# Performance work log

Measured on AMD Instinct MI355X. Metric: run time of the kernel, lower is better.

Reference implementation:

```python
import jax, jax.numpy as jnp
import numpy as np

D = 1024      # input_dim == attention_dim == num_heads*head_dim
H = 16        # num_heads
HD = 64       # head_dim
FF = 4096     # ff_dim
EPS = 1e-5


def _layernorm(x, gamma, beta):
    mu = jnp.mean(x, axis=-1, keepdims=True)
    var = jnp.var(x, axis=-1, keepdims=True)
    return (x - mu) * jax.lax.rsqrt(var + EPS) * gamma + beta


def setup_inputs() -> dict:
    key = jax.random.key(0)
    ks = jax.random.split(key, 11)
    s_in = 1.0 / np.sqrt(D)
    s_ff = 1.0 / np.sqrt(FF)
    return {
        "x": jax.random.normal(ks[0], (2, 2048, D), dtype=jnp.float32),
        "w_qkv": jax.random.uniform(ks[1], (D, 3 * D), jnp.float32, -s_in, s_in),
        "b_qkv": jax.random.uniform(ks[2], (3 * D,), jnp.float32, -s_in, s_in),
        "w_o": jax.random.uniform(ks[3], (D, D), jnp.float32, -s_in, s_in),
        "b_o": jax.random.uniform(ks[4], (D,), jnp.float32, -s_in, s_in),
        "g1": jnp.ones((D,), jnp.float32),
        "be1": jnp.zeros((D,), jnp.float32),
        "w1": jax.random.uniform(ks[5], (D, FF), jnp.float32, -s_in, s_in),
        "b1": jax.random.uniform(ks[6], (FF,), jnp.float32, -s_in, s_in),
        "w2": jax.random.uniform(ks[7], (FF, D), jnp.float32, -s_ff, s_ff),
        "b2": jax.random.uniform(ks[8], (D,), jnp.float32, -s_ff, s_ff),
        "g2": jnp.ones((D,), jnp.float32),
        "be2": jnp.zeros((D,), jnp.float32),
    }


def reference(x, w_qkv, b_qkv, w_o, b_o, g1, be1, w1, b1, w2, b2, g2, be2):
    N, L, _ = x.shape
    qkv = x @ w_qkv + b_qkv                       # [N, L, 3D]
    q = qkv[..., :D].reshape(N, L, H, HD)
    k = qkv[..., D:2 * D].reshape(N, L, H, HD)
    v = qkv[..., 2 * D:].reshape(N, L, H, HD)
    scores = jnp.einsum('nqhd,nkhd->nhqk', q, k) / np.sqrt(HD)
    attn = jax.nn.softmax(scores, axis=-1)        # [N, H, L, L]
    out = jnp.einsum('nhql,nlhd->nqhd', attn, v).reshape(N, L, D)
    attn_out = out @ w_o + b_o
    # dropout is identity in eval mode
    h = _layernorm(attn_out + x, g1, be1)
    ff = jax.nn.relu(h @ w1 + b1) @ w2 + b2
    return _layernorm(h + ff, g2, be2)
```

## Files before the change

kernel.cpp:

```cpp
#include <hip/hip_runtime.h>
#include <cstddef>
#include <cstdint>

static constexpr int Dm   = 1024;
static constexpr int Hh   = 16;
static constexpr int HDd  = 64;
static constexpr int FFd  = 4096;
static constexpr int Ls   = 2048;
static constexpr int Nb   = 2;
static constexpr int Mrows = Nb * Ls;

typedef short bf16x8 __attribute__((ext_vector_type(8)));
typedef float f32x4  __attribute__((ext_vector_type(4)));

__device__ __forceinline__ ushort f2b(float f) {
    uint32_t u = __builtin_bit_cast(uint32_t, f);
    u = (u + 0x7FFFu + ((u >> 16) & 1u)) >> 16;
    return (ushort)u;
}
__device__ __forceinline__ ushort f2bf(float f) {
    return (ushort)((__builtin_bit_cast(uint32_t, f) + 0x8000u) >> 16);
}
__device__ __forceinline__ float b2f(ushort b) {
    return __builtin_bit_cast(float, (uint32_t)b << 16);
}

__device__ __forceinline__ void gl2lds16(const ushort* g, ushort* l) {
    __builtin_amdgcn_global_load_lds(
        (const __attribute__((address_space(1))) void*)g,
        (__attribute__((address_space(3))) void*)l, 16, 0, 0);
}

__global__ __launch_bounds__(256) void convert_bf16(
    const float* __restrict__ src, ushort* __restrict__ dst, int n)
{
    int i = (blockIdx.x * 256 + threadIdx.x) * 4;
    if (i >= n) return;
    float4 v = *(const float4*)(src + i);
    uint2 o;
    o.x = (uint32_t)f2b(v.x) | ((uint32_t)f2b(v.y) << 16);
    o.y = (uint32_t)f2b(v.z) | ((uint32_t)f2b(v.w) << 16);
    *(uint2*)(dst + i) = o;
}

__global__ __launch_bounds__(256) void transpose_bf16(
    const float* __restrict__ src, ushort* __restrict__ dst, int K, int N)
{
    __shared__ float t[32][33];
    const int k0 = blockIdx.y * 32, n0 = blockIdx.x * 32;
    const int tx = threadIdx.x & 31, ty = threadIdx.x >> 5;
    #pragma unroll
    for (int i = 0; i < 4; ++i)
        t[ty + i * 8][tx] = src[(size_t)(k0 + ty + i * 8) * N + n0 + tx];
    __syncthreads();
    #pragma unroll
    for (int i = 0; i < 4; ++i)
        dst[(size_t)(n0 + ty + i * 8) * K + k0 + tx] = f2b(t[tx][ty + i * 8]);
}

template <int TN, int RELU, int BF16OUT, int VOUT>
__global__ __launch_bounds__(256) void gemm_mfma(
    const ushort* __restrict__ A, const ushort* __restrict__ Bt,
    const float* __restrict__ bias, float* __restrict__ C,
    ushort* __restrict__ Cb, ushort* __restrict__ vT, int M, int N, int K)
{
    constexpr int NT = TN / 32;
    __shared__ __align__(16) ushort As[128 * 32];
    __shared__ __align__(16) ushort Bs[TN * 32];

    const int tid  = threadIdx.x;
    const int bm   = blockIdx.y * 128, bn = blockIdx.x * TN;
    const int wave = tid >> 6, lane = tid & 63;
    const int wm = (wave & 1) * 64;
    const int wn = (wave >> 1) * (TN / 2);
    const int lr = lane & 15, lq = lane >> 4;

    const int rr = wave * 16 + (lane >> 2);
    const int sg = lane & 3;
    const ushort* Ag = A  + (size_t)(bm + rr) * K + sg * 8;
    const ushort* Bg = Bt + (size_t)(bn + rr) * K + sg * 8;
    ushort* AsW = As + wave * 512;
    ushort* BsW = Bs + wave * 512;

    f32x4 acc[4][NT];
    #pragma unroll
    for (int i = 0; i < 4; ++i)
        #pragma unroll
        for (int j = 0; j < NT; ++j)
            acc[i][j] = (f32x4){0.f, 0.f, 0.f, 0.f};

    for (int k0 = 0; k0 < K; k0 += 32) {
        __syncthreads();
        gl2lds16(Ag + k0,                  AsW);
        gl2lds16(Ag + k0 + (size_t)64 * K, AsW + 2048);
        gl2lds16(Bg + k0,                  BsW);
        if (TN == 128)
            gl2lds16(Bg + k0 + (size_t)64 * K, BsW + 2048);
        __syncthreads();

        bf16x8 af[4], bf[NT];
        #pragma unroll
        for (int mt = 0; mt < 4; ++mt)
            af[mt] = *(const bf16x8*)(As + (wm + mt * 16 + lr) * 32 + lq * 8);
        #pragma unroll
        for (int nt = 0; nt < NT; ++nt)
            bf[nt] = *(const bf16x8*)(Bs + (wn + nt * 16 + lr) * 32 + lq * 8);

        #pragma unroll
        for (int mt = 0; mt < 4; ++mt)
            #pragma unroll
            for (int nt = 0; nt < NT; ++nt)
                acc[mt][nt] = __builtin_amdgcn_mfma_f32_16x16x32_bf16(
                    af[mt], bf[nt], acc[mt][nt], 0, 0, 0);
    }

    if (VOUT && bn >= 2 * Dm) {
        #pragma unroll
        for (int nt = 0; nt < NT; ++nt) {
            const int n = bn + wn + nt * 16 + lr;
            const float bv = bias[n];
            const int col = n - 2 * Dm;
            const int h = col >> 6, d = col & 63;
            #pragma unroll
            for (int mt = 0; mt < 4; ++mt) {
                const int m0 = bm + wm + mt * 16 + lq * 4;
                const int batch = m0 >> 11, key0 = m0 & (Ls - 1);
                ushort4 ob;
                ushort* op = (ushort*)&ob;
                #pragma unroll
                for (int r = 0; r < 4; ++r) op[r] = f2bf(acc[mt][nt][r] + bv);
                *(ushort4*)(vT + (((size_t)(batch * Hh + h)) * HDd + d) * Ls + key0) = ob;
            }
        }
        return;
    }
    #pragma unroll
    for (int nt = 0; nt < NT; ++nt) {
        const int n = bn + wn + nt * 16 + lr;
        const float bv = bias[n];
        #pragma unroll
        for (int mt = 0; mt < 4; ++mt) {
            const int m0 = bm + wm + mt * 16 + lq * 4;
            #pragma unroll
            for (int r = 0; r < 4; ++r) {
                float v = acc[mt][nt][r] + bv;
                if (RELU) v = fmaxf(v, 0.0f);
                if (BF16OUT) Cb[(size_t)(m0 + r) * N + n] = f2bf(v);
                else         C [(size_t)(m0 + r) * N + n] = v;
            }
        }
    }
}

__global__ __launch_bounds__(256) void attn_mfma(
    const ushort* __restrict__ qkv, const ushort* __restrict__ vT,
    ushort* __restrict__ out)
{
    const int tid = threadIdx.x, wave = tid >> 6, lane = tid & 63;
    const int lr = lane & 15, lq = lane >> 4;
    const int h = blockIdx.y, n = blockIdx.z;
    const int q0 = blockIdx.x * 64 + wave * 16;
    const size_t RS = 3 * Dm;
    const ushort* base  = qkv + (size_t)n * Ls * RS;
    const ushort* vbase = vT + (size_t)(n * Hh + h) * HDd * Ls;

    __shared__ __align__(16) ushort Kb[64 * 72];
    __shared__ __align__(16) ushort Vt[64 * 72];
    __shared__ __align__(16) ushort Pq[4][16 * 72];

    bf16x8 qf[2];
    {
        const float c = 0.18033688011112042f;
        const ushort* qg = base + (size_t)(q0 + lr) * RS + h * HDd + lq * 8;
        bf16x8 t0 = *(const bf16x8*)(qg);
        bf16x8 t1 = *(const bf16x8*)(qg + 32);
        #pragma unroll
        for (int j = 0; j < 8; ++j) {
            qf[0][j] = (short)f2b(b2f((ushort)t0[j]) * c);
            qf[1][j] = (short)f2b(b2f((ushort)t1[j]) * c);
        }
    }

    f32x4 o[4];
    #pragma unroll
    for (int dt = 0; dt < 4; ++dt) o[dt] = (f32x4){0.f, 0.f, 0.f, 0.f};
    float lpart = 0.f;

    const int srow = tid >> 2, ssg = tid & 3;
    const ushort* kg = base + (size_t)srow * RS + Dm + h * HDd;
    const ushort* vg = vbase + (size_t)srow * Ls;
    ushort* Pw = Pq[wave];

    for (int kt = 0; kt < Ls; kt += 64) {
        const ushort* kp = kg + (size_t)kt * RS;
        const ushort* vp = vg + kt;
        int4 ka = *(const int4*)(kp + ssg * 8);
        int4 kb = *(const int4*)(kp + (ssg + 4) * 8);
        int4 va = *(const int4*)(vp + ssg * 8);
        int4 vb = *(const int4*)(vp + (ssg + 4) * 8);

        __syncthreads();
        *(int4*)(Kb + srow * 72 + ssg * 8)       = ka;
        *(int4*)(Kb + srow * 72 + (ssg + 4) * 8) = kb;
        *(int4*)(Vt + srow * 72 + ssg * 8)       = va;
        *(int4*)(Vt + srow * 72 + (ssg + 4) * 8) = vb;
        __syncthreads();

        f32x4 s[4];
        #pragma unroll
        for (int mt = 0; mt < 4; ++mt) s[mt] = (f32x4){0.f, 0.f, 0.f, 0.f};
        #pragma unroll
        for (int ks = 0; ks < 2; ++ks)
            #pragma unroll
            for (int mt = 0; mt < 4; ++mt) {
                bf16x8 kf = *(const bf16x8*)(Kb + (mt * 16 + lr) * 72 + ks * 32 + lq * 8);
                s[mt] = __builtin_amdgcn_mfma_f32_16x16x32_bf16(kf, qf[ks], s[mt], 0, 0, 0);
            }

        ushort4 pb[4];
        #pragma unroll
        for (int mt = 0; mt < 4; ++mt) {
            ushort* pw = (ushort*)&pb[mt];
            #pragma unroll
            for (int r = 0; r < 4; ++r) {
                float p = exp2f(s[mt][r]);
                lpart += p;
                pw[r] = f2bf(p);
            }
        }

        #pragma unroll
        for (int mt = 0; mt < 4; ++mt)
            *(ushort4*)(Pw + lr * 72 + mt * 16 + lq * 4) = pb[mt];

        #pragma unroll
        for (int ks = 0; ks < 2; ++ks) {
            bf16x8 pf = *(const bf16x8*)(Pw + lr * 72 + ks * 32 + lq * 8);
            #pragma unroll
            for (int dt = 0; dt < 4; ++dt) {
                bf16x8 vf = *(const bf16x8*)(Vt + (dt * 16 + lr) * 72 + ks * 32 + lq * 8);
                o[dt] = __builtin_amdgcn_mfma_f32_16x16x32_bf16(vf, pf, o[dt], 0, 0, 0);
            }
        }
    }

    float lrun = lpart;
    lrun += __shfl_xor(lrun, 16);
    lrun += __shfl_xor(lrun, 32);

    const float inv = 1.0f / lrun;
    ushort* orow = out + (size_t)(n * Ls + q0 + lr) * Dm + h * HDd;
    #pragma unroll
    for (int dt = 0; dt < 4; ++dt) {
        ushort4 ob;
        ushort* op = (ushort*)&ob;
        #pragma unroll
        for (int r = 0; r < 4; ++r) op[r] = f2bf(o[dt][r] * inv);
        *(ushort4*)(orow + dt * 16 + lq * 4) = ob;
    }
}

template <int B_BF16, int OUT_F32>
__global__ __launch_bounds__(256) void add_ln(
    const float* __restrict__ a, const void* __restrict__ b,
    const float* __restrict__ gamma, const float* __restrict__ beta,
    float* __restrict__ outf, ushort* __restrict__ outb)
{
    const int row = blockIdx.x;
    const int tid = threadIdx.x;

    const float4 va = ((const float4*)(a + (size_t)row * Dm))[tid];
    float vb[4];
    if (B_BF16) {
        ushort4 u = ((const ushort4*)((const ushort*)b + (size_t)row * Dm))[tid];
        vb[0] = b2f(u.x); vb[1] = b2f(u.y); vb[2] = b2f(u.z); vb[3] = b2f(u.w);
    } else {
        float4 f = ((const float4*)((const float*)b + (size_t)row * Dm))[tid];
        vb[0] = f.x; vb[1] = f.y; vb[2] = f.z; vb[3] = f.w;
    }
    float v[4] = {va.x + vb[0], va.y + vb[1], va.z + vb[2], va.w + vb[3]};

    float s  = v[0] + v[1] + v[2] + v[3];
    float sq = v[0]*v[0] + v[1]*v[1] + v[2]*v[2] + v[3]*v[3];

    __shared__ float red[8];
    #pragma unroll
    for (int off = 32; off > 0; off >>= 1) {
        s  += __shfl_down(s, off);
        sq += __shfl_down(sq, off);
    }
    const int wv = tid >> 6;
    if ((tid & 63) == 0) { red[wv] = s; red[4 + wv] = sq; }
    __syncthreads();
    s  = red[0] + red[1] + red[2] + red[3];
    sq = red[4] + red[5] + red[6] + red[7];

    const float mu  = s * (1.0f / Dm);
    const float var = sq * (1.0f / Dm) - mu * mu;
    const float inv = rsqrtf(var + 1e-5f);

    const float4 g  = ((const float4*)gamma)[tid];
    const float4 be = ((const float4*)beta)[tid];
    float ov[4];
    ov[0] = (v[0] - mu) * inv * g.x + be.x;
    ov[1] = (v[1] - mu) * inv * g.y + be.y;
    ov[2] = (v[2] - mu) * inv * g.z + be.z;
    ov[3] = (v[3] - mu) * inv * g.w + be.w;
    if (OUT_F32) {
        float4 o4 = {ov[0], ov[1], ov[2], ov[3]};
        ((float4*)(outf + (size_t)row * Dm))[tid] = o4;
    } else {
        uint2 ob;
        ob.x = (uint32_t)f2bf(ov[0]) | ((uint32_t)f2bf(ov[1]) << 16);
        ob.y = (uint32_t)f2bf(ov[2]) | ((uint32_t)f2bf(ov[3]) << 16);
        *(uint2*)(outb + (size_t)row * Dm + tid * 4) = ob;
    }
}

extern "C" void kernel_launch(void* const* d_in, const int* in_sizes, int n_in,
                              void* d_out, int out_size, void* d_ws, size_t ws_size,
                              hipStream_t stream)
{
    const float* x     = (const float*)d_in[0];
    const float* w_qkv = (const float*)d_in[1];
    const float* b_qkv = (const float*)d_in[2];
    const float* w_o   = (const float*)d_in[3];
    const float* b_o   = (const float*)d_in[4];
    const float* g1    = (const float*)d_in[5];
    const float* be1   = (const float*)d_in[6];
    const float* w1    = (const float*)d_in[7];
    const float* b1    = (const float*)d_in[8];
    const float* w2    = (const float*)d_in[9];
    const float* b2    = (const float*)d_in[10];
    const float* g2    = (const float*)d_in[11];
    const float* be2   = (const float*)d_in[12];
    float* out = (float*)d_out;

    char* p = (char*)d_ws;
    ushort* qkvb  = (ushort*)p;  p += (size_t)Mrows * 3 * Dm * 2;
    ushort* attnb = (ushort*)p;  p += (size_t)Mrows * Dm * 2;
    float*  proj  = (float*)p;   p += (size_t)Mrows * Dm * 4;
    ushort* hb    = (ushort*)p;  p += (size_t)Mrows * Dm * 2;
    ushort* ffb   = (ushort*)p;  p += (size_t)Mrows * FFd * 2;
    ushort* xb    = (ushort*)p;  p += (size_t)Mrows * Dm * 2;
    ushort* wqkvT = (ushort*)p;  p += (size_t)(3 * Dm) * Dm * 2;
    ushort* woT   = (ushort*)p;  p += (size_t)Dm * Dm * 2;
    ushort* w1T   = (ushort*)p;  p += (size_t)FFd * Dm * 2;
    ushort* w2T   = (ushort*)p;  p += (size_t)Dm * FFd * 2;
    ushort* vTg   = (ushort*)p;  p += (size_t)Mrows * Dm * 2;

    convert_bf16<<<dim3(Mrows * Dm / 1024), dim3(256), 0, stream>>>(x, xb, Mrows * Dm);
    transpose_bf16<<<dim3(3 * Dm / 32, Dm / 32), dim3(256), 0, stream>>>(w_qkv, wqkvT, Dm, 3 * Dm);
    transpose_bf16<<<dim3(Dm / 32, Dm / 32),     dim3(256), 0, stream>>>(w_o, woT, Dm, Dm);
    transpose_bf16<<<dim3(FFd / 32, Dm / 32),    dim3(256), 0, stream>>>(w1, w1T, Dm, FFd);
    transpose_bf16<<<dim3(Dm / 32, FFd / 32),    dim3(256), 0, stream>>>(w2, w2T, FFd, Dm);

    gemm_mfma<128, 0, 1, 1><<<dim3(3 * Dm / 128, Mrows / 128), dim3(256), 0, stream>>>(
        xb, wqkvT, b_qkv, nullptr, qkvb, vTg, Mrows, 3 * Dm, Dm);

    attn_mfma<<<dim3(Ls / 64, Hh, Nb), dim3(256), 0, stream>>>(qkvb, vTg, attnb);

    gemm_mfma<64, 0, 0, 0><<<dim3(Dm / 64, Mrows / 128), dim3(256), 0, stream>>>(
        attnb, woT, b_o, proj, nullptr, nullptr, Mrows, Dm, Dm);

    add_ln<0, 0><<<dim3(Mrows), dim3(256), 0, stream>>>(proj, x, g1, be1, nullptr, hb);

    gemm_mfma<128, 1, 1, 0><<<dim3(FFd / 128, Mrows / 128), dim3(256), 0, stream>>>(
        hb, w1T, b1, nullptr, ffb, nullptr, Mrows, FFd, Dm);

    gemm_mfma<64, 0, 0, 0><<<dim3(Dm / 64, Mrows / 128), dim3(256), 0, stream>>>(
        ffb, w2T, b2, proj, nullptr, nullptr, Mrows, Dm, FFd);

    add_ln<1, 1><<<dim3(Mrows), dim3(256), 0, stream>>>(proj, hb, g2, be2, out, nullptr);
}
```

Measured before the change: 428.7 us.

## Double-buffer GEMM LDS tiles and emit bf16 projection outputs

The GEMM kernel now keeps two LDS stages. It issues the async global-to-LDS loads for the next K-slice before computing on the current one, which removes one barrier per iteration and overlaps memory latency with MFMA work. The output-projection and FFN2 GEMMs now write bf16 instead of fp32, and add_ln gains a bf16 A-input path to read them. This cuts write and read traffic for the two intermediate buffers, but doubles LDS use per block and lowers the precision of the pre-LayerNorm residual sums.

```diff
diff --git a/kernel.cpp b/kernel.cpp
--- a/kernel.cpp
+++ b/kernel.cpp
@@ -58,15 +58,16 @@
         dst[(size_t)(n0 + ty + i * 8) * K + k0 + tx] = f2b(t[tx][ty + i * 8]);
 }
 
-template <int TN, int RELU, int BF16OUT, int VOUT>
+template <int TN, int RELU, int VOUT>
 __global__ __launch_bounds__(256) void gemm_mfma(
     const ushort* __restrict__ A, const ushort* __restrict__ Bt,
-    const float* __restrict__ bias, float* __restrict__ C,
+    const float* __restrict__ bias,
     ushort* __restrict__ Cb, ushort* __restrict__ vT, int M, int N, int K)
 {
-    constexpr int NT = TN / 32;
-    __shared__ __align__(16) ushort As[128 * 32];
-    __shared__ __align__(16) ushort Bs[TN * 32];
+    constexpr int NT  = TN / 32;
+    constexpr int BSZ = TN * 32;
+    __shared__ __align__(16) ushort As[2 * 128 * 32];
+    __shared__ __align__(16) ushort Bs[2 * BSZ];
 
     const int tid  = threadIdx.x;
     const int bm   = blockIdx.y * 128, bn = blockIdx.x * TN;
@@ -79,8 +80,6 @@
     const int sg = lane & 3;
     const ushort* Ag = A  + (size_t)(bm + rr) * K + sg * 8;
     const ushort* Bg = Bt + (size_t)(bn + rr) * K + sg * 8;
-    ushort* AsW = As + wave * 512;
-    ushort* BsW = Bs + wave * 512;
 
     f32x4 acc[4][NT];
     #pragma unroll
@@ -89,22 +88,33 @@
         for (int j = 0; j < NT; ++j)
             acc[i][j] = (f32x4){0.f, 0.f, 0.f, 0.f};
 
-    for (int k0 = 0; k0 < K; k0 += 32) {
+    gl2lds16(Ag,                  As + wave * 512);
+    gl2lds16(Ag + (size_t)64 * K, As + 2048 + wave * 512);
+    gl2lds16(Bg,                  Bs + wave * 512);
+    if (TN == 128)
+        gl2lds16(Bg + (size_t)64 * K, Bs + 2048 + wave * 512);
+
+    int ib = 0;
+    for (int k0 = 0; k0 < K; k0 += 32, ib ^= 1) {
         __syncthreads();
-        gl2lds16(Ag + k0,                  AsW);
-        gl2lds16(Ag + k0 + (size_t)64 * K, AsW + 2048);
-        gl2lds16(Bg + k0,                  BsW);
-        if (TN == 128)
-            gl2lds16(Bg + k0 + (size_t)64 * K, BsW + 2048);
-        __syncthreads();
-
+        if (k0 + 32 < K) {
+            const int nb = ib ^ 1;
+            gl2lds16(Ag + k0 + 32,                  As + nb * 4096 + wave * 512);
+            gl2lds16(Ag + k0 + 32 + (size_t)64 * K, As + nb * 4096 + 2048 + wave * 512);
+            gl2lds16(Bg + k0 + 32,                  Bs + nb * BSZ + wave * 512);
+            if (TN == 128)
+                gl2lds16(Bg + k0 + 32 + (size_t)64 * K, Bs + nb * BSZ + 2048 + wave * 512);
+        }
+
+        const ushort* Ar = As + ib * 4096;
+        const ushort* Br = Bs + ib * BSZ;
         bf16x8 af[4], bf[NT];
         #pragma unroll
         for (int mt = 0; mt < 4; ++mt)
-            af[mt] = *(const bf16x8*)(As + (wm + mt * 16 + lr) * 32 + lq * 8);
+            af[mt] = *(const bf16x8*)(Ar + (wm + mt * 16 + lr) * 32 + lq * 8);
         #pragma unroll
         for (int nt = 0; nt < NT; ++nt)
-            bf[nt] = *(const bf16x8*)(Bs + (wn + nt * 16 + lr) * 32 + lq * 8);
+            bf[nt] = *(const bf16x8*)(Br + (wn + nt * 16 + lr) * 32 + lq * 8);
 
         #pragma unroll
         for (int mt = 0; mt < 4; ++mt)
@@ -145,8 +155,7 @@
             for (int r = 0; r < 4; ++r) {
                 float v = acc[mt][nt][r] + bv;
                 if (RELU) v = fmaxf(v, 0.0f);
-                if (BF16OUT) Cb[(size_t)(m0 + r) * N + n] = f2bf(v);
-                else         C [(size_t)(m0 + r) * N + n] = v;
+                Cb[(size_t)(m0 + r) * N + n] = f2bf(v);
             }
         }
     }
@@ -260,17 +269,23 @@
     }
 }
 
-template <int B_BF16, int OUT_F32>
+template <int A_BF16, int B_BF16, int OUT_F32>
 __global__ __launch_bounds__(256) void add_ln(
-    const float* __restrict__ a, const void* __restrict__ b,
+    const void* __restrict__ a, const void* __restrict__ b,
     const float* __restrict__ gamma, const float* __restrict__ beta,
     float* __restrict__ outf, ushort* __restrict__ outb)
 {
     const int row = blockIdx.x;
     const int tid = threadIdx.x;
 
-    const float4 va = ((const float4*)(a + (size_t)row * Dm))[tid];
-    float vb[4];
+    float va[4], vb[4];
+    if (A_BF16) {
+        ushort4 u = ((const ushort4*)((const ushort*)a + (size_t)row * Dm))[tid];
+        va[0] = b2f(u.x); va[1] = b2f(u.y); va[2] = b2f(u.z); va[3] = b2f(u.w);
+    } else {
+        float4 f = ((const float4*)((const float*)a + (size_t)row * Dm))[tid];
+        va[0] = f.x; va[1] = f.y; va[2] = f.z; va[3] = f.w;
+    }
     if (B_BF16) {
         ushort4 u = ((const ushort4*)((const ushort*)b + (size_t)row * Dm))[tid];
         vb[0] = b2f(u.x); vb[1] = b2f(u.y); vb[2] = b2f(u.z); vb[3] = b2f(u.w);
@@ -278,7 +293,7 @@
         float4 f = ((const float4*)((const float*)b + (size_t)row * Dm))[tid];
         vb[0] = f.x; vb[1] = f.y; vb[2] = f.z; vb[3] = f.w;
     }
-    float v[4] = {va.x + vb[0], va.y + vb[1], va.z + vb[2], va.w + vb[3]};
+    float v[4] = {va[0] + vb[0], va[1] + vb[1], va[2] + vb[2], va[3] + vb[3]};
 
     float s  = v[0] + v[1] + v[2] + v[3];
     float sq = v[0]*v[0] + v[1]*v[1] + v[2]*v[2] + v[3]*v[3];
@@ -339,9 +354,10 @@
     char* p = (char*)d_ws;
     ushort* qkvb  = (ushort*)p;  p += (size_t)Mrows * 3 * Dm * 2;
     ushort* attnb = (ushort*)p;  p += (size_t)Mrows * Dm * 2;
-    float*  proj  = (float*)p;   p += (size_t)Mrows * Dm * 4;
+    ushort* projb = (ushort*)p;  p += (size_t)Mrows * Dm * 2;
     ushort* hb    = (ushort*)p;  p += (size_t)Mrows * Dm * 2;
     ushort* ffb   = (ushort*)p;  p += (size_t)Mrows * FFd * 2;
+    ushort* ff2b  = (ushort*)p;  p += (size_t)Mrows * Dm * 2;
     ushort* xb    = (ushort*)p;  p += (size_t)Mrows * Dm * 2;
     ushort* wqkvT = (ushort*)p;  p += (size_t)(3 * Dm) * Dm * 2;
     ushort* woT   = (ushort*)p;  p += (size_t)Dm * Dm * 2;
@@ -355,21 +371,21 @@
     transpose_bf16<<<dim3(FFd / 32, Dm / 32),    dim3(256), 0, stream>>>(w1, w1T, Dm, FFd);
     transpose_bf16<<<dim3(Dm / 32, FFd / 32),    dim3(256), 0, stream>>>(w2, w2T, FFd, Dm);
 
-    gemm_mfma<128, 0, 1, 1><<<dim3(3 * Dm / 128, Mrows / 128), dim3(256), 0, stream>>>(
-        xb, wqkvT, b_qkv, nullptr, qkvb, vTg, Mrows, 3 * Dm, Dm);
+    gemm_mfma<128, 0, 1><<<dim3(3 * Dm / 128, Mrows / 128), dim3(256), 0, stream>>>(
+        xb, wqkvT, b_qkv, qkvb, vTg, Mrows, 3 * Dm, Dm);
 
     attn_mfma<<<dim3(Ls / 64, Hh, Nb), dim3(256), 0, stream>>>(qkvb, vTg, attnb);
 
-    gemm_mfma<64, 0, 0, 0><<<dim3(Dm / 64, Mrows / 128), dim3(256), 0, stream>>>(
-        attnb, woT, b_o, proj, nullptr, nullptr, Mrows, Dm, Dm);
-
-    add_ln<0, 0><<<dim3(Mrows), dim3(256), 0, stream>>>(proj, x, g1, be1, nullptr, hb);
-
-    gemm_mfma<128, 1, 1, 0><<<dim3(FFd / 128, Mrows / 128), dim3(256), 0, stream>>>(
-        hb, w1T, b1, nullptr, ffb, nullptr, Mrows, FFd, Dm);
-
-    gemm_mfma<64, 0, 0, 0><<<dim3(Dm / 64, Mrows / 128), dim3(256), 0, stream>>>(
-        ffb, w2T, b2, proj, nullptr, nullptr, Mrows, Dm, FFd);
-
-    add_ln<1, 1><<<dim3(Mrows), dim3(256), 0, stream>>>(proj, hb, g2, be2, out, nullptr);
-}
+    gemm_mfma<64, 0, 0><<<dim3(Dm / 64, Mrows / 128), dim3(256), 0, stream>>>(
+        attnb, woT, b_o, projb, nullptr, Mrows, Dm, Dm);
+
+    add_ln<1, 0, 0><<<dim3(Mrows), dim3(256), 0, stream>>>(projb, x, g1, be1, nullptr, hb);
+
+    gemm_mfma<128, 1, 0><<<dim3(FFd / 128, Mrows / 128), dim3(256), 0, stream>>>(
+        hb, w1T, b1, ffb, nullptr, Mrows, FFd, Dm);
+
+    gemm_mfma<64, 0, 0><<<dim3(Dm / 64, Mrows / 128), dim3(256), 0, stream>>>(
+        ffb, w2T, b2, ff2b, nullptr, Mrows, Dm, FFd);
+
+    add_ln<1, 1, 1><<<dim3(Mrows), dim3(256), 0, stream>>>(ff2b, hb, g2, be2, out, nullptr);
+}
```

New measurement: 408.8 us. 1.05x faster.
